# Optimization experiments

Measured on AMD Instinct MI355X. Metric: run time of the kernel, lower is better.

## Reference

```python
import jax, jax.numpy as jnp
import numpy as np

N = 50000      # number of nodes
E = 800000     # number of edges (avg degree 16)
DIN = 128
DOUT = 128
EPS = 1e-06


def setup_inputs() -> dict:
    key = jax.random.key(0)
    ks = jax.random.split(key, 10)
    scale = 1.0 / np.sqrt(DIN)
    return {
        "mean": jax.random.normal(ks[0], (N, DIN), dtype=jnp.float32),
        "var": jax.random.uniform(ks[1], (N, DIN), dtype=jnp.float32),
        "W_mean": jax.random.normal(ks[2], (DIN, DOUT), dtype=jnp.float32) * scale,
        "b_mean": jax.random.normal(ks[3], (DOUT,), dtype=jnp.float32) * scale,
        "W_var": jax.random.normal(ks[4], (DIN, DOUT), dtype=jnp.float32) * scale,
        "b_var": jax.random.normal(ks[5], (DOUT,), dtype=jnp.float32) * scale,
        "adj0_w": jax.random.uniform(ks[6], (E,), dtype=jnp.float32),
        "adj1_w": jax.random.uniform(ks[7], (E,), dtype=jnp.float32),
        "edge_src": jax.random.randint(ks[8], (E,), 0, N, dtype=jnp.int32),
        "edge_dst": jax.random.randint(ks[9], (E,), 0, N, dtype=jnp.int32),
    }


def reference(mean, var, W_mean, b_mean, W_var, b_var, adj0_w, adj1_w, edge_src, edge_dst):
    # Dense projections (dropout is identity in eval mode)
    m = jax.nn.elu(mean @ W_mean + b_mean)            # [N, DOUT]
    v = jax.nn.relu(var @ W_var + b_var) + EPS        # [N, DOUT]
    # Elementwise attention gate
    att = jnp.exp(-v)
    m = m * att
    v = v * att * att
    # SpMM aggregation: out[dst] += w * x[src]  (COO edge list)
    n = mean.shape[0]
    out_m = jax.ops.segment_sum(adj0_w[:, None] * m[edge_src], edge_dst, num_segments=n)
    out_v = jax.ops.segment_sum(adj1_w[:, None] * v[edge_src], edge_dst, num_segments=n)
    return out_m, out_v
```

## Files before the change

kernel.cpp:

```cpp
#include <hip/hip_runtime.h>
#include <hip/hip_bf16.h>
#include <math.h>

#define N_NODES 50000
#define DIN     128
#define DOUT    128
#define EPS_    1e-6f
#define N_WAVES 3125
#define NBKT    196
#define EPB     4096
#define SLOT_CAP 5120
#define NB_PROJ 782

typedef __attribute__((ext_vector_type(8))) short  bf16x8;
typedef __attribute__((ext_vector_type(4))) float  f32x4;
typedef unsigned short ushort_t;

__device__ __forceinline__ ushort_t f2bf(float f) {
    unsigned u = __float_as_uint(f);
    return (ushort_t)((u + 0x7fffu + ((u >> 16) & 1u)) >> 16);
}
__device__ __forceinline__ float bflo(unsigned u) { return __uint_as_float(u << 16); }
__device__ __forceinline__ float bfhi(unsigned u) { return __uint_as_float(u & 0xffff0000u); }

__global__ __launch_bounds__(256) void prep_w_kernel(
    const float* __restrict__ Wm, const float* __restrict__ Wv,
    ushort_t* __restrict__ fm, ushort_t* __restrict__ fv,
    int* __restrict__ gcur)
{
    const int gid = blockIdx.x * 256 + threadIdx.x;
    if (gid < NBKT) gcur[gid] = 0;
    const int k = gid >> 7, n = gid & 127;
    const int ct = n >> 4, kk = k >> 5, quad = (k >> 3) & 3, j = k & 7;
    const int idx = ((ct * 4 + kk) * 64 + quad * 16 + (n & 15)) * 8 + j;
    fm[idx] = f2bf(Wm[gid]);
    fv[idx] = f2bf(Wv[gid]);
}

__global__ __launch_bounds__(256) void fused_projA_kernel(
    const float* __restrict__ mean, const float* __restrict__ var,
    const float* __restrict__ bm,   const float* __restrict__ bv,
    const ushort_t* __restrict__ wfm, const ushort_t* __restrict__ wfv,
    ushort_t* __restrict__ mv,
    const int* __restrict__ src, const int* __restrict__ dst,
    const float* __restrict__ w0, const float* __restrict__ w1,
    int* __restrict__ gcur, uint2* __restrict__ slots, int E, int nA)
{
    if ((int)blockIdx.x < nA) {
        __shared__ uint2 s_rec[EPB];
        __shared__ int   s_gpos[EPB];
        __shared__ int   s_hist[256];
        __shared__ int   s_scn[256];
        __shared__ int   s_cur[256];
        __shared__ int   s_base[256];

        const int t  = threadIdx.x;
        const int e0 = blockIdx.x * EPB;
        const int n  = min(EPB, E - e0);

        s_hist[t] = 0;
        __syncthreads();

        int   myb[16];
        uint2 myr[16];
#pragma unroll
        for (int j = 0; j < 16; ++j) {
            const int e = e0 + t + j * 256;
            if (e < E) {
                const int d = dst[e];
                const int b = d >> 8;
                myb[j] = b;
                myr[j].x = (unsigned)src[e] | ((unsigned)(d & 255) << 16);
                myr[j].y = (unsigned)f2bf(w0[e]) | ((unsigned)f2bf(w1[e]) << 16);
                atomicAdd(&s_hist[b], 1);
            } else myb[j] = -1;
        }
        __syncthreads();

        if (t < NBKT) {
            const int c = s_hist[t];
            s_base[t] = t * SLOT_CAP + (c ? atomicAdd(&gcur[t], c) : 0);
        }
        const int x = s_hist[t];
        s_scn[t] = x;
        __syncthreads();
        for (int off = 1; off < 256; off <<= 1) {
            const int v = (t >= off) ? s_scn[t - off] : 0;
            __syncthreads();
            s_scn[t] += v;
            __syncthreads();
        }
        const int excl = s_scn[t] - x;
        __syncthreads();
        s_scn[t] = excl;
        s_cur[t] = 0;
        __syncthreads();

#pragma unroll
        for (int j = 0; j < 16; ++j) {
            if (myb[j] >= 0) {
                const int r = atomicAdd(&s_cur[myb[j]], 1);
                const int p = s_scn[myb[j]] + r;
                s_rec[p]  = myr[j];
                s_gpos[p] = s_base[myb[j]] + r;
            }
        }
        __syncthreads();

        for (int i = t; i < n; i += 256)
            slots[s_gpos[i]] = s_rec[i];
        return;
    }

    const int wave = ((int)blockIdx.x - nA) * 4 + (threadIdx.x >> 6);
    if (wave >= N_WAVES) return;
    const int lane = threadIdx.x & 63;
    const int row0 = wave * 16;
    const int kq   = lane >> 4;
    const int arow = row0 + (lane & 15);

    f32x4 accm[8], accv[8];
#pragma unroll
    for (int ct = 0; ct < 8; ++ct) {
        accm[ct] = (f32x4){0.f, 0.f, 0.f, 0.f};
        accv[ct] = (f32x4){0.f, 0.f, 0.f, 0.f};
    }

    const float* mrow = mean + (size_t)arow * DIN;
    const float* vrow = var  + (size_t)arow * DIN;

#pragma unroll
    for (int kk = 0; kk < 4; ++kk) {
        const int kb = kk * 32 + kq * 8;
        const float4 am0 = *(const float4*)(mrow + kb);
        const float4 am1 = *(const float4*)(mrow + kb + 4);
        const float4 av0 = *(const float4*)(vrow + kb);
        const float4 av1 = *(const float4*)(vrow + kb + 4);
        bf16x8 a_m, a_v;
        a_m[0]=f2bf(am0.x); a_m[1]=f2bf(am0.y); a_m[2]=f2bf(am0.z); a_m[3]=f2bf(am0.w);
        a_m[4]=f2bf(am1.x); a_m[5]=f2bf(am1.y); a_m[6]=f2bf(am1.z); a_m[7]=f2bf(am1.w);
        a_v[0]=f2bf(av0.x); a_v[1]=f2bf(av0.y); a_v[2]=f2bf(av0.z); a_v[3]=f2bf(av0.w);
        a_v[4]=f2bf(av1.x); a_v[5]=f2bf(av1.y); a_v[6]=f2bf(av1.z); a_v[7]=f2bf(av1.w);

#pragma unroll
        for (int ct = 0; ct < 8; ++ct) {
            const bf16x8 b_m = *(const bf16x8*)(wfm + ((size_t)(ct * 4 + kk) * 64 + lane) * 8);
            const bf16x8 b_v = *(const bf16x8*)(wfv + ((size_t)(ct * 4 + kk) * 64 + lane) * 8);
            accm[ct] = __builtin_amdgcn_mfma_f32_16x16x32_bf16(a_m, b_m, accm[ct], 0, 0, 0);
            accv[ct] = __builtin_amdgcn_mfma_f32_16x16x32_bf16(a_v, b_v, accv[ct], 0, 0, 0);
        }
    }

#pragma unroll
    for (int ct = 0; ct < 8; ++ct) {
        const int col = ct * 16 + (lane & 15);
        const float bmc = bm[col];
        const float bvc = bv[col];
        const int pbase = (col >> 1) * 4 + (col & 1);
#pragma unroll
        for (int r = 0; r < 4; ++r) {
            const int row = row0 + kq * 4 + r;
            float m = accm[ct][r] + bmc;
            m = (m > 0.0f) ? m : (expf(m) - 1.0f);
            float v = accv[ct][r] + bvc;
            v = ((v > 0.0f) ? v : 0.0f) + EPS_;
            const float att = expf(-v);
            ushort_t* rowp = mv + (size_t)row * 256;
            rowp[pbase]     = f2bf(m * att);
            rowp[pbase + 2] = f2bf(v * att * att);
        }
    }
}

__global__ __launch_bounds__(256) void bucketB_kernel(
    const int* __restrict__ gcur,
    const uint2* __restrict__ slots, uint2* __restrict__ final_e,
    int* __restrict__ node_start)
{
    __shared__ int s_hist[256];
    __shared__ int s_scn[256];
    __shared__ int s_cur[256];
    __shared__ int s_red[256];

    const int b = blockIdx.x;
    const int t = threadIdx.x;

    s_red[t]  = (t < b) ? gcur[t] : 0;
    s_hist[t] = 0;
    __syncthreads();
    for (int off = 128; off > 0; off >>= 1) {
        if (t < off) s_red[t] += s_red[t + off];
        __syncthreads();
    }
    const int base = s_red[0];
    const int cnt  = gcur[b];
    const uint2* slot = slots + (size_t)b * SLOT_CAP;

    for (int i = t; i < cnt; i += 256)
        atomicAdd(&s_hist[(slot[i].x >> 16) & 255], 1);
    __syncthreads();

    const int x = s_hist[t];
    s_scn[t] = x;
    __syncthreads();
    for (int off = 1; off < 256; off <<= 1) {
        const int v = (t >= off) ? s_scn[t - off] : 0;
        __syncthreads();
        s_scn[t] += v;
        __syncthreads();
    }
    const int excl = s_scn[t] - x;
    __syncthreads();

    const int gidx = b * 256 + t;
    if (gidx <= N_NODES) node_start[gidx] = base + excl;

    s_cur[t] = excl;
    __syncthreads();

    for (int i = t; i < cnt; i += 256) {
        const uint2 r = slot[i];
        const int f = (r.x >> 16) & 255;
        const int p = atomicAdd(&s_cur[f], 1);
        final_e[base + p] = r;
    }
}

#define PAIR_FMA(RW, G) do {                                                 \
    const float a0 = bflo(RW), a1 = bfhi(RW);                                \
    am0 = fmaf(a0, bflo((G).x), am0); am1 = fmaf(a0, bfhi((G).x), am1);      \
    av0 = fmaf(a1, bflo((G).y), av0); av1 = fmaf(a1, bfhi((G).y), av1);      \
    am2 = fmaf(a0, bflo((G).z), am2); am3 = fmaf(a0, bfhi((G).z), am3);      \
    av2 = fmaf(a1, bflo((G).w), av2); av3 = fmaf(a1, bfhi((G).w), av3);      \
} while (0)

__global__ __launch_bounds__(256) void agg_kernel(
    const ushort_t* __restrict__ mv,
    const uint2* __restrict__ edges, const int* __restrict__ node_start,
    float* __restrict__ out_m, float* __restrict__ out_v)
{
    const int node = blockIdx.x * 4 + (threadIdx.x >> 6);
    const int lane = threadIdx.x & 63;
    const int half = lane >> 5;
    const int l    = lane & 31;
    if (node >= N_NODES) return;

    const int j0 = node_start[node];
    const int j1 = node_start[node + 1];

    float am0=0.f, am1=0.f, am2=0.f, am3=0.f;
    float av0=0.f, av1=0.f, av2=0.f, av3=0.f;

    int j = j0;

    if ((j & 1) && j < j1) {
        const uint2 r = edges[j];
        const unsigned rw = half ? 0u : r.y;
        const uint4 g = *(const uint4*)(mv + (size_t)(r.x & 0xffffu) * 256 + l * 8);
        PAIR_FMA(rw, g);
        ++j;
    }

    for (; j + 8 <= j1; j += 8) {
        const uint4 e0 = *(const uint4*)(edges + j + 0);
        const uint4 e1 = *(const uint4*)(edges + j + 2);
        const uint4 e2 = *(const uint4*)(edges + j + 4);
        const uint4 e3 = *(const uint4*)(edges + j + 6);
        const unsigned s0 = half ? e0.z : e0.x, w0 = half ? e0.w : e0.y;
        const unsigned s1 = half ? e1.z : e1.x, w1 = half ? e1.w : e1.y;
        const unsigned s2 = half ? e2.z : e2.x, w2 = half ? e2.w : e2.y;
        const unsigned s3 = half ? e3.z : e3.x, w3 = half ? e3.w : e3.y;
        const uint4 g0 = *(const uint4*)(mv + (size_t)(s0 & 0xffffu) * 256 + l * 8);
        const uint4 g1 = *(const uint4*)(mv + (size_t)(s1 & 0xffffu) * 256 + l * 8);
        const uint4 g2 = *(const uint4*)(mv + (size_t)(s2 & 0xffffu) * 256 + l * 8);
        const uint4 g3 = *(const uint4*)(mv + (size_t)(s3 & 0xffffu) * 256 + l * 8);
        PAIR_FMA(w0, g0);
        PAIR_FMA(w1, g1);
        PAIR_FMA(w2, g2);
        PAIR_FMA(w3, g3);
    }

    for (; j + 2 <= j1; j += 2) {
        const uint4 e = *(const uint4*)(edges + j);
        const unsigned s = half ? e.z : e.x, w = half ? e.w : e.y;
        const uint4 g = *(const uint4*)(mv + (size_t)(s & 0xffffu) * 256 + l * 8);
        PAIR_FMA(w, g);
    }

    if (j < j1) {
        const uint2 r = edges[j];
        const unsigned rw = half ? 0u : r.y;
        const uint4 g = *(const uint4*)(mv + (size_t)(r.x & 0xffffu) * 256 + l * 8);
        PAIR_FMA(rw, g);
    }

    am0 += __shfl_xor(am0, 32); am1 += __shfl_xor(am1, 32);
    am2 += __shfl_xor(am2, 32); am3 += __shfl_xor(am3, 32);
    av0 += __shfl_xor(av0, 32); av1 += __shfl_xor(av1, 32);
    av2 += __shfl_xor(av2, 32); av3 += __shfl_xor(av3, 32);

    if (half == 0) {
        *(float4*)(out_m + (size_t)node * DOUT + l * 4) = make_float4(am0, am1, am2, am3);
        *(float4*)(out_v + (size_t)node * DOUT + l * 4) = make_float4(av0, av1, av2, av3);
    }
}

extern "C" void kernel_launch(void* const* d_in, const int* in_sizes, int n_in,
                              void* d_out, int out_size, void* d_ws, size_t ws_size,
                              hipStream_t stream) {
    const float* mean = (const float*)d_in[0];
    const float* var  = (const float*)d_in[1];
    const float* Wm   = (const float*)d_in[2];
    const float* bm   = (const float*)d_in[3];
    const float* Wv   = (const float*)d_in[4];
    const float* bv   = (const float*)d_in[5];
    const float* a0   = (const float*)d_in[6];
    const float* a1   = (const float*)d_in[7];
    const int*   es   = (const int*)d_in[8];
    const int*   ed   = (const int*)d_in[9];
    const int    E    = in_sizes[6];

    char* ws = (char*)d_ws;
    ushort_t* mv        = (ushort_t*)ws;
    uint2* slots        = (uint2*)(ws + 25600000);
    uint2* final_e      = (uint2*)(ws + 33628160);
    int*   node_start   = (int*)  (ws + 40028160);
    int*   gcur         = (int*)  (ws + 40228176);
    ushort_t* wfm       = (ushort_t*)(ws + 40228976);
    ushort_t* wfv       = wfm + 16384;

    float* out_m = (float*)d_out;
    float* out_v = out_m + (size_t)N_NODES * DOUT;

    prep_w_kernel<<<64, 256, 0, stream>>>(Wm, Wv, wfm, wfv, gcur);

    const int nA = (E + EPB - 1) / EPB;
    fused_projA_kernel<<<nA + NB_PROJ, 256, 0, stream>>>(
        mean, var, bm, bv, wfm, wfv, mv,
        es, ed, a0, a1, gcur, slots, E, nA);

    bucketB_kernel<<<NBKT, 256, 0, stream>>>(
        gcur, slots, final_e, node_start);

    agg_kernel<<<(N_NODES + 3) / 4, 256, 0, stream>>>(
        mv, final_e, node_start, out_m, out_v);
}
```

Before: 209.6 us.

## Replace two-level bucket sort with per-node histogram, scan, and atomic scatter

Builds the CSR edge list by counting edges per destination node with global atomics, scanning the counts, and then scattering each edge into its final position via an atomic cursor per node. This removes the intermediate slot buffer and the second-level shared-memory sort in the bucket kernel. In exchange it reads the destination array twice and issues two global atomics per edge. Edge order within a node becomes nondeterministic, so floating-point sums are no longer reproducible.

```diff
diff --git a/kernel.cpp b/kernel.cpp
--- a/kernel.cpp
+++ b/kernel.cpp
@@ -6,10 +6,8 @@
 #define DIN     128
 #define DOUT    128
 #define EPS_    1e-6f
-#define N_WAVES 3125
 #define NBKT    196
 #define EPB     4096
-#define SLOT_CAP 5120
 #define NB_PROJ 782
 
 typedef __attribute__((ext_vector_type(8))) short  bf16x8;
@@ -26,94 +24,50 @@
 __global__ __launch_bounds__(256) void prep_w_kernel(
     const float* __restrict__ Wm, const float* __restrict__ Wv,
     ushort_t* __restrict__ fm, ushort_t* __restrict__ fv,
-    int* __restrict__ gcur)
+    int* __restrict__ gh, int* __restrict__ gcur)
 {
     const int gid = blockIdx.x * 256 + threadIdx.x;
-    if (gid < NBKT) gcur[gid] = 0;
-    const int k = gid >> 7, n = gid & 127;
-    const int ct = n >> 4, kk = k >> 5, quad = (k >> 3) & 3, j = k & 7;
-    const int idx = ((ct * 4 + kk) * 64 + quad * 16 + (n & 15)) * 8 + j;
-    fm[idx] = f2bf(Wm[gid]);
-    fv[idx] = f2bf(Wv[gid]);
-}
-
-__global__ __launch_bounds__(256) void fused_projA_kernel(
+    if (gid < N_NODES) gh[gid] = 0;
+    if (gid < NBKT)    gcur[gid] = 0;
+    if (gid < DIN * DOUT) {
+        const int k = gid >> 7, n = gid & 127;
+        const int ct = n >> 4, kk = k >> 5, quad = (k >> 3) & 3, j = k & 7;
+        const int idx = ((ct * 4 + kk) * 64 + quad * 16 + (n & 15)) * 8 + j;
+        fm[idx] = f2bf(Wm[gid]);
+        fv[idx] = f2bf(Wv[gid]);
+    }
+}
+
+__global__ __launch_bounds__(256) void fused_projH_kernel(
     const float* __restrict__ mean, const float* __restrict__ var,
     const float* __restrict__ bm,   const float* __restrict__ bv,
     const ushort_t* __restrict__ wfm, const ushort_t* __restrict__ wfv,
     ushort_t* __restrict__ mv,
-    const int* __restrict__ src, const int* __restrict__ dst,
-    const float* __restrict__ w0, const float* __restrict__ w1,
-    int* __restrict__ gcur, uint2* __restrict__ slots, int E, int nA)
-{
-    if ((int)blockIdx.x < nA) {
-        __shared__ uint2 s_rec[EPB];
-        __shared__ int   s_gpos[EPB];
-        __shared__ int   s_hist[256];
-        __shared__ int   s_scn[256];
-        __shared__ int   s_cur[256];
-        __shared__ int   s_base[256];
-
+    const int* __restrict__ dst, int* __restrict__ gh, int* __restrict__ gcur,
+    int E, int nH)
+{
+    if ((int)blockIdx.x < nH) {
+        __shared__ int s_h[256];
         const int t  = threadIdx.x;
         const int e0 = blockIdx.x * EPB;
-        const int n  = min(EPB, E - e0);
-
-        s_hist[t] = 0;
-        __syncthreads();
-
-        int   myb[16];
-        uint2 myr[16];
+        s_h[t] = 0;
+        __syncthreads();
 #pragma unroll
         for (int j = 0; j < 16; ++j) {
             const int e = e0 + t + j * 256;
             if (e < E) {
                 const int d = dst[e];
-                const int b = d >> 8;
-                myb[j] = b;
-                myr[j].x = (unsigned)src[e] | ((unsigned)(d & 255) << 16);
-                myr[j].y = (unsigned)f2bf(w0[e]) | ((unsigned)f2bf(w1[e]) << 16);
-                atomicAdd(&s_hist[b], 1);
-            } else myb[j] = -1;
-        }
-        __syncthreads();
-
-        if (t < NBKT) {
-            const int c = s_hist[t];
-            s_base[t] = t * SLOT_CAP + (c ? atomicAdd(&gcur[t], c) : 0);
-        }
-        const int x = s_hist[t];
-        s_scn[t] = x;
-        __syncthreads();
-        for (int off = 1; off < 256; off <<= 1) {
-            const int v = (t >= off) ? s_scn[t - off] : 0;
-            __syncthreads();
-            s_scn[t] += v;
-            __syncthreads();
-        }
-        const int excl = s_scn[t] - x;
-        __syncthreads();
-        s_scn[t] = excl;
-        s_cur[t] = 0;
-        __syncthreads();
-
-#pragma unroll
-        for (int j = 0; j < 16; ++j) {
-            if (myb[j] >= 0) {
-                const int r = atomicAdd(&s_cur[myb[j]], 1);
-                const int p = s_scn[myb[j]] + r;
-                s_rec[p]  = myr[j];
-                s_gpos[p] = s_base[myb[j]] + r;
+                atomicAdd(&gh[d], 1);
+                atomicAdd(&s_h[d >> 8], 1);
             }
         }
         __syncthreads();
-
-        for (int i = t; i < n; i += 256)
-            slots[s_gpos[i]] = s_rec[i];
+        if (t < NBKT && s_h[t]) atomicAdd(&gcur[t], s_h[t]);
         return;
     }
 
-    const int wave = ((int)blockIdx.x - nA) * 4 + (threadIdx.x >> 6);
-    if (wave >= N_WAVES) return;
+    const int wave = ((int)blockIdx.x - nH) * 4 + (threadIdx.x >> 6);
+    if (wave >= 3125) return;
     const int lane = threadIdx.x & 63;
     const int row0 = wave * 16;
     const int kq   = lane >> 4;
@@ -172,57 +126,55 @@
     }
 }
 
-__global__ __launch_bounds__(256) void bucketB_kernel(
-    const int* __restrict__ gcur,
-    const uint2* __restrict__ slots, uint2* __restrict__ final_e,
-    int* __restrict__ node_start)
-{
-    __shared__ int s_hist[256];
+__global__ __launch_bounds__(256) void scan_kernel(
+    const int* __restrict__ gh, const int* __restrict__ gcur,
+    int* __restrict__ node_start, int* __restrict__ ncur)
+{
+    __shared__ int s_red[256];
     __shared__ int s_scn[256];
-    __shared__ int s_cur[256];
-    __shared__ int s_red[256];
-
     const int b = blockIdx.x;
     const int t = threadIdx.x;
 
-    s_red[t]  = (t < b) ? gcur[t] : 0;
-    s_hist[t] = 0;
+    s_red[t] = (t < b) ? gcur[t] : 0;
+    const int gidx = b * 256 + t;
+    const int x = (gidx < N_NODES) ? gh[gidx] : 0;
+    s_scn[t] = x;
     __syncthreads();
+
     for (int off = 128; off > 0; off >>= 1) {
         if (t < off) s_red[t] += s_red[t + off];
         __syncthreads();
     }
     const int base = s_red[0];
-    const int cnt  = gcur[b];
-    const uint2* slot = slots + (size_t)b * SLOT_CAP;
-
-    for (int i = t; i < cnt; i += 256)
-        atomicAdd(&s_hist[(slot[i].x >> 16) & 255], 1);
-    __syncthreads();
-
-    const int x = s_hist[t];
-    s_scn[t] = x;
-    __syncthreads();
+
     for (int off = 1; off < 256; off <<= 1) {
         const int v = (t >= off) ? s_scn[t - off] : 0;
         __syncthreads();
         s_scn[t] += v;
         __syncthreads();
     }
-    const int excl = s_scn[t] - x;
-    __syncthreads();
-
-    const int gidx = b * 256 + t;
-    if (gidx <= N_NODES) node_start[gidx] = base + excl;
-
-    s_cur[t] = excl;
-    __syncthreads();
-
-    for (int i = t; i < cnt; i += 256) {
-        const uint2 r = slot[i];
-        const int f = (r.x >> 16) & 255;
-        const int p = atomicAdd(&s_cur[f], 1);
-        final_e[base + p] = r;
+    const int ns = base + s_scn[t] - x;
+    if (gidx <= N_NODES) node_start[gidx] = ns;
+    if (gidx <  N_NODES) ncur[gidx] = ns;
+}
+
+__global__ __launch_bounds__(256) void scatter_kernel(
+    const int* __restrict__ src, const int* __restrict__ dst,
+    const float* __restrict__ w0, const float* __restrict__ w1,
+    int* __restrict__ ncur, uint2* __restrict__ final_e, int E)
+{
+    const int e0 = blockIdx.x * 2048 + threadIdx.x;
+#pragma unroll
+    for (int j = 0; j < 8; ++j) {
+        const int e = e0 + j * 256;
+        if (e < E) {
+            const int d = dst[e];
+            uint2 r;
+            r.x = (unsigned)src[e];
+            r.y = (unsigned)f2bf(w0[e]) | ((unsigned)f2bf(w1[e]) << 16);
+            const int p = atomicAdd(&ncur[d], 1);
+            final_e[p] = r;
+        }
     }
 }
 
@@ -322,25 +274,28 @@
 
     char* ws = (char*)d_ws;
     ushort_t* mv        = (ushort_t*)ws;
-    uint2* slots        = (uint2*)(ws + 25600000);
-    uint2* final_e      = (uint2*)(ws + 33628160);
-    int*   node_start   = (int*)  (ws + 40028160);
-    int*   gcur         = (int*)  (ws + 40228176);
-    ushort_t* wfm       = (ushort_t*)(ws + 40228976);
+    uint2* final_e      = (uint2*)(ws + 25600000);
+    int*   node_start   = (int*)  (ws + 32000000);
+    int*   ncur         = (int*)  (ws + 32200016);
+    int*   gh           = (int*)  (ws + 32400032);
+    int*   gcur         = (int*)  (ws + 32600048);
+    ushort_t* wfm       = (ushort_t*)(ws + 32600832);
     ushort_t* wfv       = wfm + 16384;
 
     float* out_m = (float*)d_out;
     float* out_v = out_m + (size_t)N_NODES * DOUT;
 
-    prep_w_kernel<<<64, 256, 0, stream>>>(Wm, Wv, wfm, wfv, gcur);
-
-    const int nA = (E + EPB - 1) / EPB;
-    fused_projA_kernel<<<nA + NB_PROJ, 256, 0, stream>>>(
+    prep_w_kernel<<<(N_NODES + 255) / 256, 256, 0, stream>>>(Wm, Wv, wfm, wfv, gh, gcur);
+
+    const int nH = (E + EPB - 1) / EPB;
+    fused_projH_kernel<<<nH + NB_PROJ, 256, 0, stream>>>(
         mean, var, bm, bv, wfm, wfv, mv,
-        es, ed, a0, a1, gcur, slots, E, nA);
-
-    bucketB_kernel<<<NBKT, 256, 0, stream>>>(
-        gcur, slots, final_e, node_start);
+        ed, gh, gcur, E, nH);
+
+    scan_kernel<<<NBKT, 256, 0, stream>>>(gh, gcur, node_start, ncur);
+
+    scatter_kernel<<<(E + 2047) / 2048, 256, 0, stream>>>(
+        es, ed, a0, a1, ncur, final_e, E);
 
     agg_kernel<<<(N_NODES + 3) / 4, 256, 0, stream>>>(
         mv, final_e, node_start, out_m, out_v);
```

Result: slower. 266.0 us (+26.9%).

## Count per-node degrees globally and pack projection output into 32-bit stores

Applied to the files above, without the earlier changes.

Phase A now increments a global per-node degree histogram with atomics and encodes the bucket id in each edge record. This removes the shared gpos array and halves edges per block. The second bucketing pass can then skip its histogram re-read of slots and scan the global counts directly. The projection epilogue swaps bf16 values with the neighbouring lane so it writes packed 32-bit words instead of 16-bit scattered stores. The cost is about 800K extra global atomics and a larger prep kernel that zeroes the histogram.

```diff
diff --git a/kernel.cpp b/kernel.cpp
--- a/kernel.cpp
+++ b/kernel.cpp
@@ -8,8 +8,9 @@
 #define EPS_    1e-6f
 #define N_WAVES 3125
 #define NBKT    196
-#define EPB     4096
-#define SLOT_CAP 5120
+#define EPB     2048
+#define EPT     8
+#define SLOT_CAP 4992
 #define NB_PROJ 782
 
 typedef __attribute__((ext_vector_type(8))) short  bf16x8;
@@ -26,15 +27,18 @@
 __global__ __launch_bounds__(256) void prep_w_kernel(
     const float* __restrict__ Wm, const float* __restrict__ Wv,
     ushort_t* __restrict__ fm, ushort_t* __restrict__ fv,
-    int* __restrict__ gcur)
+    int* __restrict__ gcur, int* __restrict__ gh)
 {
     const int gid = blockIdx.x * 256 + threadIdx.x;
-    if (gid < NBKT) gcur[gid] = 0;
-    const int k = gid >> 7, n = gid & 127;
-    const int ct = n >> 4, kk = k >> 5, quad = (k >> 3) & 3, j = k & 7;
-    const int idx = ((ct * 4 + kk) * 64 + quad * 16 + (n & 15)) * 8 + j;
-    fm[idx] = f2bf(Wm[gid]);
-    fv[idx] = f2bf(Wv[gid]);
+    if (gid < N_NODES) gh[gid] = 0;
+    if (gid < NBKT)    gcur[gid] = 0;
+    if (gid < DIN * DOUT) {
+        const int k = gid >> 7, n = gid & 127;
+        const int ct = n >> 4, kk = k >> 5, quad = (k >> 3) & 3, j = k & 7;
+        const int idx = ((ct * 4 + kk) * 64 + quad * 16 + (n & 15)) * 8 + j;
+        fm[idx] = f2bf(Wm[gid]);
+        fv[idx] = f2bf(Wv[gid]);
+    }
 }
 
 __global__ __launch_bounds__(256) void fused_projA_kernel(
@@ -44,11 +48,11 @@
     ushort_t* __restrict__ mv,
     const int* __restrict__ src, const int* __restrict__ dst,
     const float* __restrict__ w0, const float* __restrict__ w1,
-    int* __restrict__ gcur, uint2* __restrict__ slots, int E, int nA)
+    int* __restrict__ gcur, int* __restrict__ gh,
+    uint2* __restrict__ slots, int E, int nA)
 {
     if ((int)blockIdx.x < nA) {
         __shared__ uint2 s_rec[EPB];
-        __shared__ int   s_gpos[EPB];
         __shared__ int   s_hist[256];
         __shared__ int   s_scn[256];
         __shared__ int   s_cur[256];
@@ -61,18 +65,20 @@
         s_hist[t] = 0;
         __syncthreads();
 
-        int   myb[16];
-        uint2 myr[16];
-#pragma unroll
-        for (int j = 0; j < 16; ++j) {
+        int   myb[EPT];
+        uint2 myr[EPT];
+#pragma unroll
+        for (int j = 0; j < EPT; ++j) {
             const int e = e0 + t + j * 256;
             if (e < E) {
-                const int d = dst[e];
-                const int b = d >> 8;
-                myb[j] = b;
-                myr[j].x = (unsigned)src[e] | ((unsigned)(d & 255) << 16);
+                const int d   = dst[e];
+                const int bkt = d >> 8;
+                myb[j] = bkt;
+                myr[j].x = (unsigned)src[e] | ((unsigned)(d & 255) << 16)
+                         | ((unsigned)bkt << 24);
                 myr[j].y = (unsigned)f2bf(w0[e]) | ((unsigned)f2bf(w1[e]) << 16);
-                atomicAdd(&s_hist[b], 1);
+                atomicAdd(&s_hist[bkt], 1);
+                atomicAdd(&gh[d], 1);
             } else myb[j] = -1;
         }
         __syncthreads();
@@ -97,18 +103,19 @@
         __syncthreads();
 
 #pragma unroll
-        for (int j = 0; j < 16; ++j) {
+        for (int j = 0; j < EPT; ++j) {
             if (myb[j] >= 0) {
                 const int r = atomicAdd(&s_cur[myb[j]], 1);
-                const int p = s_scn[myb[j]] + r;
-                s_rec[p]  = myr[j];
-                s_gpos[p] = s_base[myb[j]] + r;
+                s_rec[s_scn[myb[j]] + r] = myr[j];
             }
         }
         __syncthreads();
 
-        for (int i = t; i < n; i += 256)
-            slots[s_gpos[i]] = s_rec[i];
+        for (int i = t; i < n; i += 256) {
+            const uint2 r = s_rec[i];
+            const int bkt = r.x >> 24;
+            slots[s_base[bkt] + (i - s_scn[bkt])] = r;
+        }
         return;
     }
 
@@ -151,12 +158,13 @@
         }
     }
 
+    const int par = lane & 1;
 #pragma unroll
     for (int ct = 0; ct < 8; ++ct) {
         const int col = ct * 16 + (lane & 15);
         const float bmc = bm[col];
         const float bvc = bv[col];
-        const int pbase = (col >> 1) * 4 + (col & 1);
+        const int dw = ct * 16 + ((lane & 15) >> 1) * 2 + par;
 #pragma unroll
         for (int r = 0; r < 4; ++r) {
             const int row = row0 + kq * 4 + r;
@@ -165,64 +173,58 @@
             float v = accv[ct][r] + bvc;
             v = ((v > 0.0f) ? v : 0.0f) + EPS_;
             const float att = expf(-v);
-            ushort_t* rowp = mv + (size_t)row * 256;
-            rowp[pbase]     = f2bf(m * att);
-            rowp[pbase + 2] = f2bf(v * att * att);
-        }
-    }
-}
-
-__global__ __launch_bounds__(256) void bucketB_kernel(
-    const int* __restrict__ gcur,
+            const unsigned um = f2bf(m * att);
+            const unsigned uv = f2bf(v * att * att);
+            const unsigned om = (unsigned)__shfl_xor((int)um, 1);
+            const unsigned ov = (unsigned)__shfl_xor((int)uv, 1);
+            const unsigned w = par ? (ov | (uv << 16)) : (um | (om << 16));
+            ((unsigned*)(mv + (size_t)row * 256))[dw] = w;
+        }
+    }
+}
+
+__global__ __launch_bounds__(256) void place_kernel(
+    const int* __restrict__ gh, const int* __restrict__ gcur,
     const uint2* __restrict__ slots, uint2* __restrict__ final_e,
     int* __restrict__ node_start)
 {
-    __shared__ int s_hist[256];
+    __shared__ int s_red[256];
     __shared__ int s_scn[256];
     __shared__ int s_cur[256];
-    __shared__ int s_red[256];
 
     const int b = blockIdx.x;
     const int t = threadIdx.x;
 
-    s_red[t]  = (t < b) ? gcur[t] : 0;
-    s_hist[t] = 0;
+    s_red[t] = (t < b) ? gcur[t] : 0;
+    const int gidx = b * 256 + t;
+    const int x = (gidx < N_NODES) ? gh[gidx] : 0;
+    s_scn[t] = x;
     __syncthreads();
+
     for (int off = 128; off > 0; off >>= 1) {
         if (t < off) s_red[t] += s_red[t + off];
         __syncthreads();
     }
     const int base = s_red[0];
-    const int cnt  = gcur[b];
-    const uint2* slot = slots + (size_t)b * SLOT_CAP;
-
-    for (int i = t; i < cnt; i += 256)
-        atomicAdd(&s_hist[(slot[i].x >> 16) & 255], 1);
-    __syncthreads();
-
-    const int x = s_hist[t];
-    s_scn[t] = x;
-    __syncthreads();
+
     for (int off = 1; off < 256; off <<= 1) {
         const int v = (t >= off) ? s_scn[t - off] : 0;
         __syncthreads();
         s_scn[t] += v;
         __syncthreads();
     }
-    const int excl = s_scn[t] - x;
+    const int ns = base + s_scn[t] - x;
+    if (gidx <= N_NODES) node_start[gidx] = ns;
+    s_cur[t] = ns;
     __syncthreads();
 
-    const int gidx = b * 256 + t;
-    if (gidx <= N_NODES) node_start[gidx] = base + excl;
-
-    s_cur[t] = excl;
-    __syncthreads();
-
+    const int cnt = gcur[b];
+    const uint2* slot = slots + (size_t)b * SLOT_CAP;
     for (int i = t; i < cnt; i += 256) {
         const uint2 r = slot[i];
         const int f = (r.x >> 16) & 255;
         const int p = atomicAdd(&s_cur[f], 1);
-        final_e[base + p] = r;
+        final_e[p] = r;
     }
 }
 
@@ -323,24 +325,25 @@
     char* ws = (char*)d_ws;
     ushort_t* mv        = (ushort_t*)ws;
     uint2* slots        = (uint2*)(ws + 25600000);
-    uint2* final_e      = (uint2*)(ws + 33628160);
-    int*   node_start   = (int*)  (ws + 40028160);
-    int*   gcur         = (int*)  (ws + 40228176);
-    ushort_t* wfm       = (ushort_t*)(ws + 40228976);
+    uint2* final_e      = (uint2*)(ws + 33427456);
+    int*   node_start   = (int*)  (ws + 39827456);
+    int*   gh           = (int*)  (ws + 40027472);
+    int*   gcur         = (int*)  (ws + 40227472);
+    ushort_t* wfm       = (ushort_t*)(ws + 40228288);
     ushort_t* wfv       = wfm + 16384;
 
     float* out_m = (float*)d_out;
     float* out_v = out_m + (size_t)N_NODES * DOUT;
 
-    prep_w_kernel<<<64, 256, 0, stream>>>(Wm, Wv, wfm, wfv, gcur);
+    prep_w_kernel<<<(N_NODES + 255) / 256, 256, 0, stream>>>(Wm, Wv, wfm, wfv, gcur, gh);
 
     const int nA = (E + EPB - 1) / EPB;
     fused_projA_kernel<<<nA + NB_PROJ, 256, 0, stream>>>(
         mean, var, bm, bv, wfm, wfv, mv,
-        es, ed, a0, a1, gcur, slots, E, nA);
-
-    bucketB_kernel<<<NBKT, 256, 0, stream>>>(
-        gcur, slots, final_e, node_start);
+        es, ed, a0, a1, gcur, gh, slots, E, nA);
+
+    place_kernel<<<NBKT, 256, 0, stream>>>(
+        gh, gcur, slots, final_e, node_start);
 
     agg_kernel<<<(N_NODES + 3) / 4, 256, 0, stream>>>(
         mv, final_e, node_start, out_m, out_v);
```

Result: slower. 245.9 us (+17.3%).
